# Performance work log

Hardware: AMD Instinct MI355X
Metric: run time of the kernel (lower is better)

Reference implementation:

```python
import jax, jax.numpy as jnp
import numpy as np

P, B, L = 32, 64, 128
E, HB, HP = 64, 128, 128   # byte emb dim, byte GRU hidden, packet GRU hidden
PE = 2 * HB                # packet embedding dim = 256
LH = 128                   # attention linear hidden
NC = 10                    # num classes


def _gru_dir(x, w_ih, w_hh, b_ih, b_hh, reverse=False):
    # x: [T, N, E_in] -> outputs [T, N, H]; PyTorch GRU gate math, h0 = 0.
    H = w_hh.shape[1]
    xg = jnp.einsum('tne,ge->tng', x, w_ih) + b_ih  # precompute input gates [T,N,3H]
    if reverse:
        xg = xg[::-1]

    def step(h, xgt):
        hg = h @ w_hh.T + b_hh
        xr, xz, xn = jnp.split(xgt, 3, axis=-1)
        hr, hz, hn = jnp.split(hg, 3, axis=-1)
        r = jax.nn.sigmoid(xr + hr)
        z = jax.nn.sigmoid(xz + hz)
        n = jnp.tanh(xn + r * hn)
        h = (1.0 - z) * n + z * h
        return h, h

    h0 = jnp.zeros((x.shape[1], H), x.dtype)
    _, ys = jax.lax.scan(step, h0, xg)
    if reverse:
        ys = ys[::-1]
    return ys


def _bigru(x, wif, whf, bif, bhf, wib, whb, bib, bhb):
    f = _gru_dir(x, wif, whf, bif, bhf, reverse=False)
    b = _gru_dir(x, wib, whb, bib, bhb, reverse=True)
    return jnp.concatenate([f, b], axis=-1)


def setup_inputs() -> dict:
    key = jax.random.key(0)
    ks = jax.random.split(key, 32)
    rn = lambda k, shp: (jax.random.normal(k, shp, dtype=jnp.float32) * 0.05)
    inp = {}
    inp['flow'] = jax.random.randint(ks[0], (P, B, L), 0, 256, dtype=jnp.int64)
    inp['emb'] = rn(ks[1], (256, E))
    # byte biGRU (forward / backward dirs)
    inp['byte_wih_f'] = rn(ks[2], (3 * HB, E)); inp['byte_whh_f'] = rn(ks[3], (3 * HB, HB))
    inp['byte_bih_f'] = rn(ks[4], (3 * HB,));   inp['byte_bhh_f'] = rn(ks[5], (3 * HB,))
    inp['byte_wih_b'] = rn(ks[6], (3 * HB, E)); inp['byte_whh_b'] = rn(ks[7], (3 * HB, HB))
    inp['byte_bih_b'] = rn(ks[8], (3 * HB,));   inp['byte_bhh_b'] = rn(ks[9], (3 * HB,))
    # packet biGRU
    inp['pkt_wih_f'] = rn(ks[10], (3 * HP, PE)); inp['pkt_whh_f'] = rn(ks[11], (3 * HP, HP))
    inp['pkt_bih_f'] = rn(ks[12], (3 * HP,));    inp['pkt_bhh_f'] = rn(ks[13], (3 * HP,))
    inp['pkt_wih_b'] = rn(ks[14], (3 * HP, PE)); inp['pkt_whh_b'] = rn(ks[15], (3 * HP, HP))
    inp['pkt_bih_b'] = rn(ks[16], (3 * HP,));    inp['pkt_bhh_b'] = rn(ks[17], (3 * HP,))
    # byte attention (Linear(2HB->LH), Linear(LH->1))
    inp['ba_w1'] = rn(ks[18], (LH, 2 * HB)); inp['ba_b1'] = rn(ks[19], (LH,))
    inp['ba_w2'] = rn(ks[20], (1, LH));      inp['ba_b2'] = rn(ks[21], (1,))
    # packet attention (Linear(2HP->LH), Linear(LH->1))
    inp['pa_w1'] = rn(ks[22], (LH, 2 * HP)); inp['pa_b1'] = rn(ks[23], (LH,))
    inp['pa_w2'] = rn(ks[24], (1, LH));      inp['pa_b2'] = rn(ks[25], (1,))
    # final classifier
    inp['wf'] = rn(ks[26], (NC, 2 * HP)); inp['bf'] = rn(ks[27], (NC,))
    return inp


def reference(flow, emb,
              byte_wih_f, byte_whh_f, byte_bih_f, byte_bhh_f,
              byte_wih_b, byte_whh_b, byte_bih_b, byte_bhh_b,
              pkt_wih_f, pkt_whh_f, pkt_bih_f, pkt_bhh_f,
              pkt_wih_b, pkt_whh_b, pkt_bih_b, pkt_bhh_b,
              ba_w1, ba_b1, ba_w2, ba_b2,
              pa_w1, pa_b1, pa_w2, pa_b2,
              wf, bf):
    p, b, l = flow.shape
    x = emb[flow]                                   # [P,B,L,E]
    # batch the per-packet byte GRU across packets: [L, P*B, E]
    xb = x.transpose(2, 0, 1, 3).reshape(l, p * b, E)
    out = _bigru(xb, byte_wih_f, byte_whh_f, byte_bih_f, byte_bhh_f,
                 byte_wih_b, byte_whh_b, byte_bih_b, byte_bhh_b)  # [L, P*B, 2HB]
    out = out.reshape(l, p, b, 2 * HB)
    # Attention: tanh(lin1) -> lin2 -> softmax over dim=1 of the [L,B,1] view,
    # i.e. over the batch axis (faithful to the original code).
    h = jnp.tanh(jnp.einsum('lpbd,hd->lpbh', out, ba_w1) + ba_b1)
    score = jnp.einsum('lpbh,oh->lpbo', h, ba_w2) + ba_b2          # [L,P,B,1]
    attn = jax.nn.softmax(score, axis=2)
    packet_emb = (out * attn).sum(axis=0)                          # [P,B,2HB]
    # packet biGRU over packet sequence
    out2 = _bigru(packet_emb, pkt_wih_f, pkt_whh_f, pkt_bih_f, pkt_bhh_f,
                  pkt_wih_b, pkt_whh_b, pkt_bih_b, pkt_bhh_b)      # [P,B,2HP]
    h2 = jnp.tanh(jnp.einsum('pbd,hd->pbh', out2, pa_w1) + pa_b1)
    score2 = jnp.einsum('pbh,oh->pbo', h2, pa_w2) + pa_b2          # [P,B,1]
    attn2 = jax.nn.softmax(score2, axis=1)
    flow_emb = (out2 * attn2).sum(axis=1)                          # [P,2HP] (faithful sum over dim=1)
    return flow_emb @ wf.T + bf                                    # [P,NC]
```

## Files before the change

kernel.cpp:

```cpp
#include <hip/hip_runtime.h>
#include <hip/hip_bf16.h>
#include <hip/hip_fp16.h>
#include <cstdint>
#include <cstddef>


#define DINLINE __device__ __forceinline__

typedef _Float16 f16;
typedef f16 f16x8 __attribute__((ext_vector_type(8)));
typedef float f32x4 __attribute__((ext_vector_type(4)));

static DINLINE float fast_sigmoid(float x) {
    const float e = __builtin_amdgcn_exp2f(-1.44269504089f * x);
    return __builtin_amdgcn_rcpf(1.0f + e);
}
static DINLINE float fast_tanh(float x) {
    const float e = __builtin_amdgcn_exp2f(2.88539008178f * x);
    return 1.0f - 2.0f * __builtin_amdgcn_rcpf(1.0f + e);
}

static DINLINE void lds_barrier() {
    asm volatile("s_waitcnt lgkmcnt(0)\n\ts_barrier" ::: "memory");
    __builtin_amdgcn_sched_barrier(0);
}

__global__ void k_tables(const float* __restrict__ emb,
                         const float* __restrict__ wihF, const float* __restrict__ bihF,
                         const float* __restrict__ bhhF,
                         const float* __restrict__ wihB, const float* __restrict__ bihB,
                         const float* __restrict__ bhhB,
                         float4* __restrict__ tab4F, float4* __restrict__ tab4B) {
    const int v = blockIdx.x & 255;
    const int dir = blockIdx.x >> 8;
    const float* wih = dir ? wihB : wihF;
    const float* bih = dir ? bihB : bihF;
    const float* bhh = dir ? bhhB : bhhF;
    float4* tab4 = dir ? tab4B : tab4F;
    __shared__ float er[64];
    __shared__ float sh[384];
    if (threadIdx.x < 64) er[threadIdx.x] = emb[v * 64 + threadIdx.x];
    __syncthreads();
    const int g = threadIdx.x;
    float acc = bih[g] + (g < 256 ? bhh[g] : 0.0f);
    #pragma unroll
    for (int e = 0; e < 64; ++e) acc = fmaf(wih[g * 64 + e], er[e], acc);
    sh[g] = acc;
    __syncthreads();
    if (g < 128) {
        float4 pk;
        pk.x = sh[g];
        pk.y = sh[g + 128];
        pk.z = sh[g + 256];
        pk.w = 0.f;
        tab4[v * 128 + g] = pk;
    }
}

__global__ void k_prep_w1(const float* __restrict__ w1, f16* __restrict__ w1h) {
    const int col = blockIdx.x;
    const int k = threadIdx.x;
    w1h[col * 256 + (k ^ ((col & 7) << 3))] = (f16)w1[col * 256 + k];
}

struct TransArgs {
    const float* src[2];
    float* dst[2];
    int R[2];
    int C[2];
};
__global__ void k_transpose(TransArgs a) {
    const int m = blockIdx.y;
    const float* __restrict__ s = a.src[m];
    float* __restrict__ d = a.dst[m];
    const int R = a.R[m], C = a.C[m];
    const int total = R * C;
    for (int idx = blockIdx.x * blockDim.x + threadIdx.x; idx < total;
         idx += gridDim.x * blockDim.x) {
        const int r = idx / C, c = idx - r * C;
        d[c * R + r] = s[idx];
    }
}

__global__ __launch_bounds__(512, 1) void k_byte_gru(
    const int* __restrict__ flow,
    const float4* __restrict__ tab4F, const float4* __restrict__ tab4B,
    const float* __restrict__ whhF, const float* __restrict__ whhB,
    const float* __restrict__ bhhF, const float* __restrict__ bhhB,
    __half* __restrict__ hF, __half* __restrict__ hB) {
    const int dir = blockIdx.x & 1;
    const int chunk = blockIdx.x >> 1;
    const int row0 = chunk * 16;
    const int tid = threadIdx.x;
    const int wid = tid >> 6;
    const int lane = tid & 63;
    const int c = lane & 15;
    const int q = lane >> 4;
    const int j = wid * 16 + c;

    const float4* __restrict__ t4 = dir ? tab4B : tab4F;
    const float* __restrict__ whh = dir ? whhB : whhF;
    const float* __restrict__ bhh = dir ? bhhB : bhhF;
    __half* __restrict__ hout = dir ? hB : hF;

    __shared__ f16 hbuf[2][16 * 128];
    __shared__ int flow_lds[16][128];

    for (int i = tid; i < 16 * 128; i += 512)
        flow_lds[i >> 7][i & 127] = flow[row0 * 128 + i] & 255;
    for (int i = tid; i < 16 * 128; i += 512) hbuf[0][i] = (f16)0.f;

    f16x8 Bf[3][4];
    #pragma unroll
    for (int g = 0; g < 3; ++g) {
        #pragma unroll
        for (int ks = 0; ks < 4; ++ks) {
            const float* src = whh + (size_t)(g * 128 + j) * 128 + ks * 32 + q * 8;
            f16x8 b;
            #pragma unroll
            for (int e = 0; e < 8; ++e) b[e] = (f16)src[e];
            Bf[g][ks] = b;
        }
    }
    const float bh2 = bhh[j + 256];
    float hold[4];
    #pragma unroll
    for (int rr = 0; rr < 4; ++rr) hold[rr] = 0.f;
    __syncthreads();

    for (int t = 0; t < 128; ++t) {
        const int curb = t & 1, nxtb = curb ^ 1;
        const int tt = dir ? (127 - t) : t;

        float4 x4[4];
        #pragma unroll
        for (int rr = 0; rr < 4; ++rr)
            x4[rr] = t4[flow_lds[q * 4 + rr][tt] * 128 + j];

        f16x8 Af[4];
        #pragma unroll
        for (int ks = 0; ks < 4; ++ks) {
            const int kb = ks * 32 + q * 8;
            const int idx = c * 128 + (kb ^ ((c & 7) << 3));
            Af[ks] = *reinterpret_cast<const f16x8*>(&hbuf[curb][idx]);
        }

        f32x4 a0 = {0.f, 0.f, 0.f, 0.f};
        f32x4 a1 = {0.f, 0.f, 0.f, 0.f};
        f32x4 a2 = {0.f, 0.f, 0.f, 0.f};
        #pragma unroll
        for (int ks = 0; ks < 4; ++ks) {
            a0 = __builtin_amdgcn_mfma_f32_16x16x32_f16(Af[ks], Bf[0][ks], a0, 0, 0, 0);
            a1 = __builtin_amdgcn_mfma_f32_16x16x32_f16(Af[ks], Bf[1][ks], a1, 0, 0, 0);
            a2 = __builtin_amdgcn_mfma_f32_16x16x32_f16(Af[ks], Bf[2][ks], a2, 0, 0, 0);
        }

        #pragma unroll
        for (int rr = 0; rr < 4; ++rr) {
            const float rg = fast_sigmoid(x4[rr].x + a0[rr]);
            const float zg = fast_sigmoid(x4[rr].y + a1[rr]);
            const float ng = fast_tanh(x4[rr].z + rg * (a2[rr] + bh2));
            const float hn = fmaf(zg, hold[rr] - ng, ng);
            hold[rr] = hn;
            const int row = q * 4 + rr;
            hbuf[nxtb][row * 128 + (j ^ ((row & 7) << 3))] = (f16)hn;
        }
        lds_barrier();

        {
            const int row = tid >> 5;
            const int ho = (tid & 31) * 4;
            const int idx = row * 128 + (ho ^ ((row & 7) << 3));
            const uint2 v = *reinterpret_cast<const uint2*>(&hbuf[nxtb][idx]);
            *reinterpret_cast<uint2*>(
                &hout[((size_t)tt * 2048 + row0 + row) * 128 + ho]) = v;
        }
    }
}

__global__ __launch_bounds__(256, 1) void k_scores_attn(
    const __half* __restrict__ hF, const __half* __restrict__ hB,
    const f16* __restrict__ w1h,
    const float* __restrict__ b1, const float* __restrict__ w2,
    const float* __restrict__ b2, float* __restrict__ attn) {
    __shared__ f16 w1lds[128 * 256];
    __shared__ float sc[128];
    const int tid = threadIdx.x;
    {
        const uint2* src = reinterpret_cast<const uint2*>(w1h);
        uint2* dst = reinterpret_cast<uint2*>(w1lds);
        for (int i = tid; i < 8192; i += 256) dst[i] = src[i];
    }
    const int lane = tid & 63, w = tid >> 6;
    const int c = lane & 15, q = lane >> 4;

    float b1v[8], w2v[8];
    #pragma unroll
    for (int ct = 0; ct < 8; ++ct) {
        b1v[ct] = b1[ct * 16 + c];
        w2v[ct] = w2[ct * 16 + c];
    }
    const float b2v = b2[0];
    __syncthreads();

    for (int it = 0; it < 4; ++it) {
        const int pos0 = blockIdx.x * 512 + it * 128;

        f16x8 Af[2][8];
        #pragma unroll
        for (int pt = 0; pt < 2; ++pt) {
            const size_t pos = (size_t)pos0 + (w * 2 + pt) * 16 + c;
            const f16* hFp = (const f16*)(hF + pos * 128);
            const f16* hBp = (const f16*)(hB + pos * 128);
            #pragma unroll
            for (int ks = 0; ks < 4; ++ks)
                Af[pt][ks] = *reinterpret_cast<const f16x8*>(hFp + ks * 32 + q * 8);
            #pragma unroll
            for (int ks = 0; ks < 4; ++ks)
                Af[pt][4 + ks] = *reinterpret_cast<const f16x8*>(hBp + ks * 32 + q * 8);
        }

        float s[2][4] = {{0.f, 0.f, 0.f, 0.f}, {0.f, 0.f, 0.f, 0.f}};
        #pragma unroll
        for (int ct = 0; ct < 8; ++ct) {
            const int jj = ct * 16 + c;
            f16x8 Bfr[8];
            #pragma unroll
            for (int ks = 0; ks < 8; ++ks) {
                const int k = ks * 32 + q * 8;
                Bfr[ks] = *reinterpret_cast<const f16x8*>(
                    &w1lds[jj * 256 + (k ^ ((jj & 7) << 3))]);
            }
            #pragma unroll
            for (int pt = 0; pt < 2; ++pt) {
                f32x4 acc = {0.f, 0.f, 0.f, 0.f};
                #pragma unroll
                for (int ks = 0; ks < 8; ++ks)
                    acc = __builtin_amdgcn_mfma_f32_16x16x32_f16(Af[pt][ks],
                                                                 Bfr[ks], acc,
                                                                 0, 0, 0);
                #pragma unroll
                for (int rr = 0; rr < 4; ++rr)
                    s[pt][rr] += w2v[ct] * fast_tanh(acc[rr] + b1v[ct]);
            }
        }
        #pragma unroll
        for (int pt = 0; pt < 2; ++pt) {
            #pragma unroll
            for (int rr = 0; rr < 4; ++rr) {
                float v = s[pt][rr];
                v += __shfl_xor(v, 1);
                v += __shfl_xor(v, 2);
                v += __shfl_xor(v, 4);
                v += __shfl_xor(v, 8);
                if (c == 0) sc[(w * 2 + pt) * 16 + q * 4 + rr] = v + b2v;
            }
        }
        __syncthreads();
        if (tid < 128) {
            const float sv = sc[tid];
            float m = sv;
            for (int off = 32; off; off >>= 1) m = fmaxf(m, __shfl_xor(m, off));
            const float e = __expf(sv - m);
            float sum = e;
            for (int off = 32; off; off >>= 1) sum += __shfl_xor(sum, off);
            attn[pos0 + tid] = e / sum;
        }
        __syncthreads();
    }
}

__global__ __launch_bounds__(256) void k_packet_emb(
    const __half* __restrict__ hF, const __half* __restrict__ hB,
    const float* __restrict__ attn, float* __restrict__ pe) {
    const int tid = threadIdx.x;
    const int w = tid >> 6;
    const int lane = tid & 63;
    const int n = blockIdx.x * 2 + (w >> 1);
    const int l0 = (w & 1) * 64;
    const bool isF = lane < 32;
    const int chunk = lane & 31;
    const __half* __restrict__ hsrc = (isF ? hF : hB) + (size_t)n * 128 + chunk * 4;
    float acc0 = 0.f, acc1 = 0.f, acc2 = 0.f, acc3 = 0.f;
    #pragma unroll 4
    for (int li = 0; li < 64; ++li) {
        const int l = l0 + li;
        const float wv = attn[l * 2048 + n];
        const uint2 u = *reinterpret_cast<const uint2*>(hsrc + (size_t)l * 2048 * 128);
        const f16* hv = reinterpret_cast<const f16*>(&u);
        acc0 = fmaf(wv, (float)hv[0], acc0);
        acc1 = fmaf(wv, (float)hv[1], acc1);
        acc2 = fmaf(wv, (float)hv[2], acc2);
        acc3 = fmaf(wv, (float)hv[3], acc3);
    }
    __shared__ float4 part[4][64];
    part[w][lane] = (float4){acc0, acc1, acc2, acc3};
    __syncthreads();
    if ((w & 1) == 0) {
        const float4 a = part[w][lane];
        const float4 b = part[w + 1][lane];
        float4 o = {a.x + b.x, a.y + b.y, a.z + b.z, a.w + b.w};
        *reinterpret_cast<float4*>(&pe[n * 256 + (isF ? 0 : 128) + chunk * 4]) = o;
    }
}

__global__ __launch_bounds__(384) void k_pkt_xg(
    const float* __restrict__ pe, const float* __restrict__ wihTF,
    const float* __restrict__ bihF, const float* __restrict__ bhhF,
    const float* __restrict__ wihTB, const float* __restrict__ bihB,
    const float* __restrict__ bhhB, float4* __restrict__ xg4F,
    float4* __restrict__ xg4B) {
    const int dir = blockIdx.y;
    const float* __restrict__ wihT = dir ? wihTB : wihTF;
    const float* __restrict__ bih = dir ? bihB : bihF;
    const float* __restrict__ bhh = dir ? bhhB : bhhF;
    float4* __restrict__ xg4 = dir ? xg4B : xg4F;
    const int rbase = blockIdx.x * 8;
    __shared__ float xrow[8][256];
    __shared__ float sh[8][384];
    for (int i = threadIdx.x; i < 8 * 256; i += 384)
        xrow[i >> 8][i & 255] = pe[rbase * 256 + i];
    __syncthreads();
    const int g = threadIdx.x;
    float acc[8];
    const float bias = bih[g] + (g < 256 ? bhh[g] : 0.0f);
    #pragma unroll
    for (int r = 0; r < 8; ++r) acc[r] = bias;
    for (int d = 0; d < 256; ++d) {
        const float w = wihT[d * 384 + g];
        #pragma unroll
        for (int r = 0; r < 8; ++r) acc[r] = fmaf(w, xrow[r][d], acc[r]);
    }
    #pragma unroll
    for (int r = 0; r < 8; ++r) sh[r][g] = acc[r];
    __syncthreads();
    for (int i = threadIdx.x; i < 8 * 128; i += 384) {
        const int r = i >> 7, jj = i & 127;
        float4 pk;
        pk.x = sh[r][jj];
        pk.y = sh[r][jj + 128];
        pk.z = sh[r][jj + 256];
        pk.w = 0.f;
        xg4[(size_t)(rbase + r) * 128 + jj] = pk;
    }
}

__global__ __launch_bounds__(512, 1) void k_pkt_gru(
    const float4* __restrict__ xg4F, const float4* __restrict__ xg4B,
    const float* __restrict__ whhF, const float* __restrict__ whhB,
    const float* __restrict__ bhhF, const float* __restrict__ bhhB,
    float* __restrict__ h2F, float* __restrict__ h2B) {
    const int dir = blockIdx.x & 1;
    const int chunk = blockIdx.x >> 1;
    const int row0 = chunk * 16;
    const int tid = threadIdx.x;
    const int wid = tid >> 6;
    const int lane = tid & 63;
    const int c = lane & 15;
    const int q = lane >> 4;
    const int j = wid * 16 + c;

    const float4* __restrict__ xg4 = dir ? xg4B : xg4F;
    const float* __restrict__ whh = dir ? whhB : whhF;
    const float* __restrict__ bhh = dir ? bhhB : bhhF;
    float* __restrict__ hout = dir ? h2B : h2F;

    __shared__ f16 hbuf[2][16 * 128];

    for (int i = tid; i < 16 * 128; i += 512) hbuf[0][i] = (f16)0.f;

    f16x8 Bf[3][4];
    #pragma unroll
    for (int g = 0; g < 3; ++g) {
        #pragma unroll
        for (int ks = 0; ks < 4; ++ks) {
            const float* src = whh + (size_t)(g * 128 + j) * 128 + ks * 32 + q * 8;
            f16x8 b;
            #pragma unroll
            for (int e = 0; e < 8; ++e) b[e] = (f16)src[e];
            Bf[g][ks] = b;
        }
    }
    const float bh2 = bhh[j + 256];
    float hold[4];
    #pragma unroll
    for (int rr = 0; rr < 4; ++rr) hold[rr] = 0.f;
    __syncthreads();

    for (int t = 0; t < 32; ++t) {
        const int curb = t & 1, nxtb = curb ^ 1;
        const int tt = dir ? (31 - t) : t;

        float4 x4[4];
        #pragma unroll
        for (int rr = 0; rr < 4; ++rr)
            x4[rr] = xg4[(size_t)(tt * 64 + row0 + q * 4 + rr) * 128 + j];

        f16x8 Af[4];
        #pragma unroll
        for (int ks = 0; ks < 4; ++ks) {
            const int kb = ks * 32 + q * 8;
            const int idx = c * 128 + (kb ^ ((c & 7) << 3));
            Af[ks] = *reinterpret_cast<const f16x8*>(&hbuf[curb][idx]);
        }

        f32x4 a0 = {0.f, 0.f, 0.f, 0.f};
        f32x4 a1 = {0.f, 0.f, 0.f, 0.f};
        f32x4 a2 = {0.f, 0.f, 0.f, 0.f};
        #pragma unroll
        for (int ks = 0; ks < 4; ++ks) {
            a0 = __builtin_amdgcn_mfma_f32_16x16x32_f16(Af[ks], Bf[0][ks], a0, 0, 0, 0);
            a1 = __builtin_amdgcn_mfma_f32_16x16x32_f16(Af[ks], Bf[1][ks], a1, 0, 0, 0);
            a2 = __builtin_amdgcn_mfma_f32_16x16x32_f16(Af[ks], Bf[2][ks], a2, 0, 0, 0);
        }

        #pragma unroll
        for (int rr = 0; rr < 4; ++rr) {
            const float rg = fast_sigmoid(x4[rr].x + a0[rr]);
            const float zg = fast_sigmoid(x4[rr].y + a1[rr]);
            const float ng = fast_tanh(x4[rr].z + rg * (a2[rr] + bh2));
            const float hn = fmaf(zg, hold[rr] - ng, ng);
            hold[rr] = hn;
            const int row = q * 4 + rr;
            hbuf[nxtb][row * 128 + (j ^ ((row & 7) << 3))] = (f16)hn;
            hout[((size_t)tt * 64 + row0 + row) * 128 + j] = hn;
        }
        lds_barrier();
    }
}

__global__ __launch_bounds__(128) void k_scores2(
    const float* __restrict__ h2F, const float* __restrict__ h2B,
    const float* __restrict__ paw1,
    const float* __restrict__ pab1, const float* __restrict__ paw2,
    const float* __restrict__ pab2, float* __restrict__ scores2) {
    const int n = blockIdx.x;
    const int tid = threadIdx.x;
    __shared__ float x[256];
    __shared__ float red[2];
    x[tid] = h2F[n * 128 + tid];
    x[tid + 128] = h2B[n * 128 + tid];
    __syncthreads();
    float acc = pab1[tid];
    const float* wr = paw1 + tid * 256;
    #pragma unroll 8
    for (int d = 0; d < 256; ++d) acc = fmaf(wr[d], x[d], acc);
    float s = paw2[tid] * fast_tanh(acc);
    s += __shfl_xor(s, 1);
    s += __shfl_xor(s, 2);
    s += __shfl_xor(s, 4);
    s += __shfl_xor(s, 8);
    s += __shfl_xor(s, 16);
    s += __shfl_xor(s, 32);
    if ((tid & 63) == 0) red[tid >> 6] = s;
    __syncthreads();
    if (tid == 0) scores2[n] = red[0] + red[1] + pab2[0];
}

__global__ __launch_bounds__(256) void k_final3(
    const float* __restrict__ h2F, const float* __restrict__ h2B,
    const float* __restrict__ scores2, const float* __restrict__ wf,
    const float* __restrict__ bfv, float* __restrict__ outp) {
    const int p = blockIdx.x;
    const int tid = threadIdx.x;
    __shared__ float sc[64];
    __shared__ float femb[256];
    __shared__ float red[64];

    if (tid < 64) {
        const float s = scores2[p * 64 + tid];
        float m = s;
        for (int off = 32; off; off >>= 1) m = fmaxf(m, __shfl_xor(m, off));
        const float e = __expf(s - m);
        float sum = e;
        for (int off = 32; off; off >>= 1) sum += __shfl_xor(sum, off);
        sc[tid] = e / sum;
    }
    __syncthreads();

    {
        const float* __restrict__ hsrc = (tid < 128) ? h2F : h2B;
        const int d = tid & 127;
        float acc = 0.f;
        for (int b = 0; b < 64; ++b)
            acc = fmaf(sc[b], hsrc[(p * 64 + b) * 128 + d], acc);
        femb[tid] = acc;
    }
    __syncthreads();

    const float fv = femb[tid];
    #pragma unroll
    for (int c = 0; c < 10; ++c) {
        float s = fv * wf[c * 256 + tid];
        s += __shfl_xor(s, 1);
        s += __shfl_xor(s, 2);
        s += __shfl_xor(s, 4);
        s += __shfl_xor(s, 8);
        s += __shfl_xor(s, 16);
        s += __shfl_xor(s, 32);
        if ((tid & 63) == 0) red[(c << 2) | (tid >> 6)] = s;
        __syncthreads();
        if (tid == 0)
            outp[p * 10 + c] = bfv[c] + red[c << 2] + red[(c << 2) | 1] +
                               red[(c << 2) | 2] + red[(c << 2) | 3];
        __syncthreads();
    }
}

extern "C" void kernel_launch(void* const* d_in, const int* in_sizes, int n_in,
                              void* d_out, int out_size, void* d_ws,
                              size_t ws_size, hipStream_t stream) {
    const int* flow = (const int*)d_in[0];
    const float* emb = (const float*)d_in[1];
    const float* byte_wih_f = (const float*)d_in[2];
    const float* byte_whh_f = (const float*)d_in[3];
    const float* byte_bih_f = (const float*)d_in[4];
    const float* byte_bhh_f = (const float*)d_in[5];
    const float* byte_wih_b = (const float*)d_in[6];
    const float* byte_whh_b = (const float*)d_in[7];
    const float* byte_bih_b = (const float*)d_in[8];
    const float* byte_bhh_b = (const float*)d_in[9];
    const float* pkt_wih_f = (const float*)d_in[10];
    const float* pkt_whh_f = (const float*)d_in[11];
    const float* pkt_bih_f = (const float*)d_in[12];
    const float* pkt_bhh_f = (const float*)d_in[13];
    const float* pkt_wih_b = (const float*)d_in[14];
    const float* pkt_whh_b = (const float*)d_in[15];
    const float* pkt_bih_b = (const float*)d_in[16];
    const float* pkt_bhh_b = (const float*)d_in[17];
    const float* ba_w1 = (const float*)d_in[18];
    const float* ba_b1 = (const float*)d_in[19];
    const float* ba_w2 = (const float*)d_in[20];
    const float* ba_b2 = (const float*)d_in[21];
    const float* pa_w1 = (const float*)d_in[22];
    const float* pa_b1 = (const float*)d_in[23];
    const float* pa_w2 = (const float*)d_in[24];
    const float* pa_b2 = (const float*)d_in[25];
    const float* wf = (const float*)d_in[26];
    const float* bf = (const float*)d_in[27];

    char* base = (char*)d_ws;
    size_t off = 0;
    auto allocf = [&](size_t nf) -> float* {
        float* p = (float*)(base + off);
        off += nf * sizeof(float);
        return p;
    };
    auto alloch = [&](size_t nh) -> __half* {
        off = (off + 255) & ~(size_t)255;
        __half* p = (__half*)(base + off);
        off += nh * sizeof(__half);
        return p;
    };
    float* wihTpF = allocf(256 * 384);
    float* wihTpB = allocf(256 * 384);
    float* attn = allocf(262144);
    float* pe = allocf(2048 * 256);
    float4* tab4F = (float4*)allocf(256 * 128 * 4);
    float4* tab4B = (float4*)allocf(256 * 128 * 4);
    float4* xg4F = (float4*)allocf((size_t)2048 * 128 * 4);
    float4* xg4B = (float4*)allocf((size_t)2048 * 128 * 4);
    float* h2F = allocf(32 * 64 * 128);
    float* h2B = allocf(32 * 64 * 128);
    float* scores2 = allocf(2048);
    __half* w1h = alloch(128 * 256);
    __half* hF = alloch((size_t)128 * 2048 * 128);
    __half* hB = alloch((size_t)128 * 2048 * 128);
    if (off > ws_size) return;
    (void)in_sizes; (void)n_in; (void)out_size;

    k_tables<<<512, 384, 0, stream>>>(emb, byte_wih_f, byte_bih_f, byte_bhh_f,
                                      byte_wih_b, byte_bih_b, byte_bhh_b,
                                      tab4F, tab4B);
    k_prep_w1<<<128, 256, 0, stream>>>(ba_w1, (f16*)w1h);

    TransArgs ta;
    ta.src[0] = pkt_wih_f; ta.dst[0] = wihTpF; ta.R[0] = 384; ta.C[0] = 256;
    ta.src[1] = pkt_wih_b; ta.dst[1] = wihTpB; ta.R[1] = 384; ta.C[1] = 256;
    k_transpose<<<dim3(96, 2), 256, 0, stream>>>(ta);

    k_byte_gru<<<256, 512, 0, stream>>>(flow, tab4F, tab4B, byte_whh_f,
                                        byte_whh_b, byte_bhh_f, byte_bhh_b, hF,
                                        hB);

    k_scores_attn<<<512, 256, 0, stream>>>(hF, hB, (const f16*)w1h, ba_b1,
                                           ba_w2, ba_b2, attn);
    k_packet_emb<<<1024, 256, 0, stream>>>(hF, hB, attn, pe);

    k_pkt_xg<<<dim3(256, 2), 384, 0, stream>>>(pe, wihTpF, pkt_bih_f,
                                               pkt_bhh_f, wihTpB, pkt_bih_b,
                                               pkt_bhh_b, xg4F, xg4B);
    k_pkt_gru<<<8, 512, 0, stream>>>(xg4F, xg4B, pkt_whh_f, pkt_whh_b,
                                     pkt_bhh_f, pkt_bhh_b, h2F, h2B);
    k_scores2<<<2048, 128, 0, stream>>>(h2F, h2B, pa_w1, pa_b1, pa_w2, pa_b2,
                                        scores2);
    k_final3<<<32, 256, 0, stream>>>(h2F, h2B, scores2, wf, bf, (float*)d_out);
}
```

Measured before the change: 294.1 us.

## Fuse packet embedding with input-gate GEMM, merge prep kernels, pad LDS rows

```diff
diff --git a/kernel.cpp b/kernel.cpp
--- a/kernel.cpp
+++ b/kernel.cpp
@@ -11,6 +11,8 @@
 typedef f16 f16x8 __attribute__((ext_vector_type(8)));
 typedef float f32x4 __attribute__((ext_vector_type(4)));
 
+#define HS 136
+
 static DINLINE float fast_sigmoid(float x) {
     const float e = __builtin_amdgcn_exp2f(-1.44269504089f * x);
     return __builtin_amdgcn_rcpf(1.0f + e);
@@ -25,12 +27,20 @@
     __builtin_amdgcn_sched_barrier(0);
 }
 
-__global__ void k_tables(const float* __restrict__ emb,
-                         const float* __restrict__ wihF, const float* __restrict__ bihF,
-                         const float* __restrict__ bhhF,
-                         const float* __restrict__ wihB, const float* __restrict__ bihB,
-                         const float* __restrict__ bhhB,
-                         float4* __restrict__ tab4F, float4* __restrict__ tab4B) {
+__global__ void k_tables_w1(const float* __restrict__ emb,
+                            const float* __restrict__ wihF, const float* __restrict__ bihF,
+                            const float* __restrict__ bhhF,
+                            const float* __restrict__ wihB, const float* __restrict__ bihB,
+                            const float* __restrict__ bhhB,
+                            float4* __restrict__ tab4F, float4* __restrict__ tab4B,
+                            const float* __restrict__ w1, f16* __restrict__ w1h) {
+    if (blockIdx.x >= 512) {
+        const int col = blockIdx.x - 512;
+        const int k = threadIdx.x;
+        if (k < 256)
+            w1h[col * 256 + (k ^ ((col & 7) << 3))] = (f16)w1[col * 256 + k];
+        return;
+    }
     const int v = blockIdx.x & 255;
     const int dir = blockIdx.x >> 8;
     const float* wih = dir ? wihB : wihF;
@@ -55,12 +65,6 @@
         pk.w = 0.f;
         tab4[v * 128 + g] = pk;
     }
-}
-
-__global__ void k_prep_w1(const float* __restrict__ w1, f16* __restrict__ w1h) {
-    const int col = blockIdx.x;
-    const int k = threadIdx.x;
-    w1h[col * 256 + (k ^ ((col & 7) << 3))] = (f16)w1[col * 256 + k];
 }
 
 struct TransArgs {
@@ -98,17 +102,21 @@
     const int q = lane >> 4;
     const int j = wid * 16 + c;
 
-    const float4* __restrict__ t4 = dir ? tab4B : tab4F;
+    const char* __restrict__ t4 =
+        reinterpret_cast<const char*>(dir ? tab4B : tab4F);
     const float* __restrict__ whh = dir ? whhB : whhF;
     const float* __restrict__ bhh = dir ? bhhB : bhhF;
     __half* __restrict__ hout = dir ? hB : hF;
 
-    __shared__ f16 hbuf[2][16 * 128];
+    __shared__ f16 hbuf[2][16 * HS];
     __shared__ int flow_lds[16][128];
 
     for (int i = tid; i < 16 * 128; i += 512)
-        flow_lds[i >> 7][i & 127] = flow[row0 * 128 + i] & 255;
-    for (int i = tid; i < 16 * 128; i += 512) hbuf[0][i] = (f16)0.f;
+        flow_lds[i >> 7][i & 127] = (flow[row0 * 128 + i] & 255) << 11;
+    {
+        f16* hb = reinterpret_cast<f16*>(hbuf);
+        for (int i = tid; i < 2 * 16 * HS; i += 512) hb[i] = (f16)0.f;
+    }
 
     f16x8 Bf[3][4];
     #pragma unroll
@@ -126,6 +134,12 @@
     float hold[4];
     #pragma unroll
     for (int rr = 0; rr < 4; ++rr) hold[rr] = 0.f;
+
+    const char* t4j = t4 + (j << 4);
+    const int abase = c * HS + q * 8;
+    const int wbase = (q * 4) * HS + j;
+    const int srow = tid >> 5;
+    const int sidx = srow * HS + (tid & 31) * 4;
     __syncthreads();
 
     for (int t = 0; t < 128; ++t) {
@@ -135,15 +149,13 @@
         float4 x4[4];
         #pragma unroll
         for (int rr = 0; rr < 4; ++rr)
-            x4[rr] = t4[flow_lds[q * 4 + rr][tt] * 128 + j];
+            x4[rr] = *reinterpret_cast<const float4*>(
+                t4j + flow_lds[q * 4 + rr][tt]);
 
         f16x8 Af[4];
         #pragma unroll
-        for (int ks = 0; ks < 4; ++ks) {
-            const int kb = ks * 32 + q * 8;
-            const int idx = c * 128 + (kb ^ ((c & 7) << 3));
-            Af[ks] = *reinterpret_cast<const f16x8*>(&hbuf[curb][idx]);
-        }
+        for (int ks = 0; ks < 4; ++ks)
+            Af[ks] = *reinterpret_cast<const f16x8*>(&hbuf[curb][abase + ks * 32]);
 
         f32x4 a0 = {0.f, 0.f, 0.f, 0.f};
         f32x4 a1 = {0.f, 0.f, 0.f, 0.f};
@@ -162,18 +174,14 @@
             const float ng = fast_tanh(x4[rr].z + rg * (a2[rr] + bh2));
             const float hn = fmaf(zg, hold[rr] - ng, ng);
             hold[rr] = hn;
-            const int row = q * 4 + rr;
-            hbuf[nxtb][row * 128 + (j ^ ((row & 7) << 3))] = (f16)hn;
+            hbuf[nxtb][wbase + rr * HS] = (f16)hn;
         }
         lds_barrier();
 
         {
-            const int row = tid >> 5;
-            const int ho = (tid & 31) * 4;
-            const int idx = row * 128 + (ho ^ ((row & 7) << 3));
-            const uint2 v = *reinterpret_cast<const uint2*>(&hbuf[nxtb][idx]);
+            const uint2 v = *reinterpret_cast<const uint2*>(&hbuf[nxtb][sidx]);
             *reinterpret_cast<uint2*>(
-                &hout[((size_t)tt * 2048 + row0 + row) * 128 + ho]) = v;
+                &hout[((size_t)tt * 2048 + row0 + srow) * 128 + (tid & 31) * 4]) = v;
         }
     }
 }
@@ -270,78 +278,74 @@
     }
 }
 
-__global__ __launch_bounds__(256) void k_packet_emb(
+__global__ __launch_bounds__(512) void k_pe_xg(
     const __half* __restrict__ hF, const __half* __restrict__ hB,
-    const float* __restrict__ attn, float* __restrict__ pe) {
+    const float* __restrict__ attn,
+    const float* __restrict__ wihTF, const float* __restrict__ bihF,
+    const float* __restrict__ bhhF,
+    const float* __restrict__ wihTB, const float* __restrict__ bihB,
+    const float* __restrict__ bhhB,
+    float4* __restrict__ xg4F, float4* __restrict__ xg4B) {
     const int tid = threadIdx.x;
-    const int w = tid >> 6;
-    const int lane = tid & 63;
-    const int n = blockIdx.x * 2 + (w >> 1);
-    const int l0 = (w & 1) * 64;
-    const bool isF = lane < 32;
-    const int chunk = lane & 31;
-    const __half* __restrict__ hsrc = (isF ? hF : hB) + (size_t)n * 128 + chunk * 4;
-    float acc0 = 0.f, acc1 = 0.f, acc2 = 0.f, acc3 = 0.f;
-    #pragma unroll 4
-    for (int li = 0; li < 64; ++li) {
-        const int l = l0 + li;
-        const float wv = attn[l * 2048 + n];
-        const uint2 u = *reinterpret_cast<const uint2*>(hsrc + (size_t)l * 2048 * 128);
-        const f16* hv = reinterpret_cast<const f16*>(&u);
-        acc0 = fmaf(wv, (float)hv[0], acc0);
-        acc1 = fmaf(wv, (float)hv[1], acc1);
-        acc2 = fmaf(wv, (float)hv[2], acc2);
-        acc3 = fmaf(wv, (float)hv[3], acc3);
-    }
-    __shared__ float4 part[4][64];
-    part[w][lane] = (float4){acc0, acc1, acc2, acc3};
-    __syncthreads();
-    if ((w & 1) == 0) {
-        const float4 a = part[w][lane];
-        const float4 b = part[w + 1][lane];
-        float4 o = {a.x + b.x, a.y + b.y, a.z + b.z, a.w + b.w};
-        *reinterpret_cast<float4*>(&pe[n * 256 + (isF ? 0 : 128) + chunk * 4]) = o;
-    }
-}
-
-__global__ __launch_bounds__(384) void k_pkt_xg(
-    const float* __restrict__ pe, const float* __restrict__ wihTF,
-    const float* __restrict__ bihF, const float* __restrict__ bhhF,
-    const float* __restrict__ wihTB, const float* __restrict__ bihB,
-    const float* __restrict__ bhhB, float4* __restrict__ xg4F,
-    float4* __restrict__ xg4B) {
-    const int dir = blockIdx.y;
-    const float* __restrict__ wihT = dir ? wihTB : wihTF;
-    const float* __restrict__ bih = dir ? bihB : bihF;
-    const float* __restrict__ bhh = dir ? bhhB : bhhF;
-    float4* __restrict__ xg4 = dir ? xg4B : xg4F;
+    const int w = tid >> 6, lane = tid & 63;
     const int rbase = blockIdx.x * 8;
+    const int n = rbase + w;
     __shared__ float xrow[8][256];
     __shared__ float sh[8][384];
-    for (int i = threadIdx.x; i < 8 * 256; i += 384)
-        xrow[i >> 8][i & 255] = pe[rbase * 256 + i];
-    __syncthreads();
-    const int g = threadIdx.x;
-    float acc[8];
-    const float bias = bih[g] + (g < 256 ? bhh[g] : 0.0f);
-    #pragma unroll
-    for (int r = 0; r < 8; ++r) acc[r] = bias;
-    for (int d = 0; d < 256; ++d) {
-        const float w = wihT[d * 384 + g];
-        #pragma unroll
-        for (int r = 0; r < 8; ++r) acc[r] = fmaf(w, xrow[r][d], acc[r]);
-    }
-    #pragma unroll
-    for (int r = 0; r < 8; ++r) sh[r][g] = acc[r];
-    __syncthreads();
-    for (int i = threadIdx.x; i < 8 * 128; i += 384) {
-        const int r = i >> 7, jj = i & 127;
-        float4 pk;
-        pk.x = sh[r][jj];
-        pk.y = sh[r][jj + 128];
-        pk.z = sh[r][jj + 256];
-        pk.w = 0.f;
-        xg4[(size_t)(rbase + r) * 128 + jj] = pk;
+
+    {
+        const bool isF = lane < 32;
+        const int chunk = lane & 31;
+        const __half* __restrict__ hsrc =
+            (isF ? hF : hB) + (size_t)n * 128 + chunk * 4;
+        float a0 = 0.f, a1 = 0.f, a2 = 0.f, a3 = 0.f;
+        #pragma unroll 4
+        for (int l = 0; l < 128; ++l) {
+            const float wv = attn[l * 2048 + n];
+            const uint2 u =
+                *reinterpret_cast<const uint2*>(hsrc + (size_t)l * 2048 * 128);
+            const f16* hv = reinterpret_cast<const f16*>(&u);
+            a0 = fmaf(wv, (float)hv[0], a0);
+            a1 = fmaf(wv, (float)hv[1], a1);
+            a2 = fmaf(wv, (float)hv[2], a2);
+            a3 = fmaf(wv, (float)hv[3], a3);
+        }
+        float4 o = {a0, a1, a2, a3};
+        *reinterpret_cast<float4*>(&xrow[w][(isF ? 0 : 128) + chunk * 4]) = o;
+    }
+    __syncthreads();
+
+    #pragma unroll
+    for (int dir = 0; dir < 2; ++dir) {
+        const float* __restrict__ wihT = dir ? wihTB : wihTF;
+        const float* __restrict__ bih = dir ? bihB : bihF;
+        const float* __restrict__ bhh = dir ? bhhB : bhhF;
+        float4* __restrict__ xg4 = dir ? xg4B : xg4F;
+        if (tid < 384) {
+            const int g = tid;
+            const float bias = bih[g] + (g < 256 ? bhh[g] : 0.0f);
+            float acc[8];
+            #pragma unroll
+            for (int r = 0; r < 8; ++r) acc[r] = bias;
+            for (int d = 0; d < 256; ++d) {
+                const float wv = wihT[d * 384 + g];
+                #pragma unroll
+                for (int r = 0; r < 8; ++r) acc[r] = fmaf(wv, xrow[r][d], acc[r]);
+            }
+            #pragma unroll
+            for (int r = 0; r < 8; ++r) sh[r][g] = acc[r];
+        }
+        __syncthreads();
+        for (int i = tid; i < 8 * 128; i += 512) {
+            const int r = i >> 7, jj = i & 127;
+            float4 pk;
+            pk.x = sh[r][jj];
+            pk.y = sh[r][jj + 128];
+            pk.z = sh[r][jj + 256];
+            pk.w = 0.f;
+            xg4[(size_t)(rbase + r) * 128 + jj] = pk;
+        }
+        __syncthreads();
     }
 }
 
@@ -365,9 +369,12 @@
     const float* __restrict__ bhh = dir ? bhhB : bhhF;
     float* __restrict__ hout = dir ? h2B : h2F;
 
-    __shared__ f16 hbuf[2][16 * 128];
-
-    for (int i = tid; i < 16 * 128; i += 512) hbuf[0][i] = (f16)0.f;
+    __shared__ f16 hbuf[2][16 * HS];
+
+    {
+        f16* hb = reinterpret_cast<f16*>(hbuf);
+        for (int i = tid; i < 2 * 16 * HS; i += 512) hb[i] = (f16)0.f;
+    }
 
     f16x8 Bf[3][4];
     #pragma unroll
@@ -385,6 +392,9 @@
     float hold[4];
     #pragma unroll
     for (int rr = 0; rr < 4; ++rr) hold[rr] = 0.f;
+
+    const int abase = c * HS + q * 8;
+    const int wbase = (q * 4) * HS + j;
     __syncthreads();
 
     for (int t = 0; t < 32; ++t) {
@@ -398,11 +408,8 @@
 
         f16x8 Af[4];
         #pragma unroll
-        for (int ks = 0; ks < 4; ++ks) {
-            const int kb = ks * 32 + q * 8;
-            const int idx = c * 128 + (kb ^ ((c & 7) << 3));
-            Af[ks] = *reinterpret_cast<const f16x8*>(&hbuf[curb][idx]);
-        }
+        for (int ks = 0; ks < 4; ++ks)
+            Af[ks] = *reinterpret_cast<const f16x8*>(&hbuf[curb][abase + ks * 32]);
 
         f32x4 a0 = {0.f, 0.f, 0.f, 0.f};
         f32x4 a1 = {0.f, 0.f, 0.f, 0.f};
@@ -421,9 +428,8 @@
             const float ng = fast_tanh(x4[rr].z + rg * (a2[rr] + bh2));
             const float hn = fmaf(zg, hold[rr] - ng, ng);
             hold[rr] = hn;
-            const int row = q * 4 + rr;
-            hbuf[nxtb][row * 128 + (j ^ ((row & 7) << 3))] = (f16)hn;
-            hout[((size_t)tt * 64 + row0 + row) * 128 + j] = hn;
+            hbuf[nxtb][wbase + rr * HS] = (f16)hn;
+            hout[((size_t)tt * 64 + row0 + q * 4 + rr) * 128 + j] = hn;
         }
         lds_barrier();
     }
@@ -555,7 +561,6 @@
     float* wihTpF = allocf(256 * 384);
     float* wihTpB = allocf(256 * 384);
     float* attn = allocf(262144);
-    float* pe = allocf(2048 * 256);
     float4* tab4F = (float4*)allocf(256 * 128 * 4);
     float4* tab4B = (float4*)allocf(256 * 128 * 4);
     float4* xg4F = (float4*)allocf((size_t)2048 * 128 * 4);
@@ -569,10 +574,10 @@
     if (off > ws_size) return;
     (void)in_sizes; (void)n_in; (void)out_size;
 
-    k_tables<<<512, 384, 0, stream>>>(emb, byte_wih_f, byte_bih_f, byte_bhh_f,
-                                      byte_wih_b, byte_bih_b, byte_bhh_b,
-                                      tab4F, tab4B);
-    k_prep_w1<<<128, 256, 0, stream>>>(ba_w1, (f16*)w1h);
+    k_tables_w1<<<640, 384, 0, stream>>>(emb, byte_wih_f, byte_bih_f,
+                                         byte_bhh_f, byte_wih_b, byte_bih_b,
+                                         byte_bhh_b, tab4F, tab4B, ba_w1,
+                                         (f16*)w1h);
 
     TransArgs ta;
     ta.src[0] = pkt_wih_f; ta.dst[0] = wihTpF; ta.R[0] = 384; ta.C[0] = 256;
@@ -585,11 +590,11 @@
 
     k_scores_attn<<<512, 256, 0, stream>>>(hF, hB, (const f16*)w1h, ba_b1,
                                            ba_w2, ba_b2, attn);
-    k_packet_emb<<<1024, 256, 0, stream>>>(hF, hB, attn, pe);
-
-    k_pkt_xg<<<dim3(256, 2), 384, 0, stream>>>(pe, wihTpF, pkt_bih_f,
-                                               pkt_bhh_f, wihTpB, pkt_bih_b,
-                                               pkt_bhh_b, xg4F, xg4B);
+
+    k_pe_xg<<<256, 512, 0, stream>>>(hF, hB, attn, wihTpF, pkt_bih_f,
+                                     pkt_bhh_f, wihTpB, pkt_bih_b, pkt_bhh_b,
+                                     xg4F, xg4B);
+
     k_pkt_gru<<<8, 512, 0, stream>>>(xg4F, xg4B, pkt_whh_f, pkt_whh_b,
                                      pkt_bhh_f, pkt_bhh_b, h2F, h2B);
     k_scores2<<<2048, 128, 0, stream>>>(h2F, h2B, pa_w1, pa_b1, pa_w2, pa_b2,
```

Measured after the change: 306.4 us. +4.2%, slower.
